# Kernel tuning notes

Hardware: AMD Instinct MI355X
Metric: run time of the kernel (lower is better)

The kernel has to match this reference:

```python
import jax, jax.numpy as jnp
import numpy as np

# geomloss SamplesLoss(loss='sinkhorn', p=2, blur=0.05):
#   cost C(x,y) = |x-y|^2 / 2, entropic eps = blur**p = 0.0025,
#   debiased divergence S = OT(x,y) - 0.5*OT(x,x) - 0.5*OT(y,y)
EPS = 0.05 ** 2          # blur**p
N_ITERS = 50             # fixed log-domain Sinkhorn iterations


def _cost(x, y):
    # x: [N,3], y: [M,3] -> [N,M] halved squared euclidean distance
    x2 = jnp.sum(x * x, axis=-1)
    y2 = jnp.sum(y * y, axis=-1)
    return 0.5 * (x2[:, None] + y2[None, :] - 2.0 * (x @ y.T))


def _ot_eps(x, y):
    # Entropic OT with uniform weights, log-domain Sinkhorn.
    N, M = x.shape[0], y.shape[0]
    logN = float(np.log(N))
    logM = float(np.log(M))
    C = _cost(x, y)  # [N,M]
    f0 = jnp.zeros((N,), dtype=x.dtype)
    g0 = jnp.zeros((M,), dtype=x.dtype)

    def step(carry, _):
        f, g = carry
        f = -EPS * (jax.nn.logsumexp((g[None, :] - C) / EPS, axis=1) - logM)
        g = -EPS * (jax.nn.logsumexp((f[:, None] - C) / EPS, axis=0) - logN)
        return (f, g), None

    (f, g), _ = jax.lax.scan(step, (f0, g0), None, length=N_ITERS)
    # OT cost at (approximate) optimal dual potentials
    return jnp.mean(f) + jnp.mean(g)


def _sinkhorn_div(x, y):
    # debiased Sinkhorn divergence per sample
    return _ot_eps(x, y) - 0.5 * _ot_eps(x, x) - 0.5 * _ot_eps(y, y)


def setup_inputs() -> dict:
    key = jax.random.key(0)
    k1, k2 = jax.random.split(key)
    B, N = 8, 2048
    pcs1 = jax.random.uniform(k1, (B, N, 3), dtype=jnp.float32)
    pcs2 = jax.random.uniform(k2, (B, N, 3), dtype=jnp.float32)
    return {"pcs1": pcs1, "pcs2": pcs2}


def reference(pcs1, pcs2):
    # mean over batch of per-sample Sinkhorn divergences
    losses = jax.vmap(_sinkhorn_div)(pcs1, pcs2)  # [B]
    return jnp.mean(losses)
```

## Files before the change

### kernel.cpp

```cpp
#include <hip/hip_runtime.h>

#ifndef __has_builtin
#define __has_builtin(x) 0
#endif

__device__ __forceinline__ float fexp2(float x) {
#if __has_builtin(__builtin_amdgcn_exp2f)
  return __builtin_amdgcn_exp2f(x);
#else
  return exp2f(x);
#endif
}
__device__ __forceinline__ float flog2(float x) {
#if __has_builtin(__builtin_amdgcn_logf)
  return __builtin_amdgcn_logf(x);
#else
  return log2f(x);
#endif
}

typedef float    f32x4 __attribute__((ext_vector_type(4)));
typedef unsigned int u32x2 __attribute__((ext_vector_type(2)));
typedef unsigned int u32x4 __attribute__((ext_vector_type(4)));
typedef _Float16 f16x4 __attribute__((ext_vector_type(4)));

__device__ __forceinline__ f32x4 mfma16x16x16(f16x4 a, f16x4 b, f32x4 c) {
#if __has_builtin(__builtin_amdgcn_mfma_f32_16x16x16_f16)
  return __builtin_amdgcn_mfma_f32_16x16x16_f16(a, b, c, 0, 0, 0);
#else
  return __builtin_amdgcn_mfma_f32_16x16x16f16(a, b, c, 0, 0, 0);
#endif
}

namespace {
constexpr int NPTS = 2048;
constexpr int NPROB = 24;
constexpr int THREADS = 512;
constexpr int NPASS = 100;
constexpr int PH = 512;
constexpr float KS  = 1.44269504088896340736f / 0.0025f;
constexpr float HKS = 0.5f * KS;
constexpr float NEG_EPS_LN2 = -0.0025f * 0.69314718055994530942f;
constexpr float LOG2N = 11.0f;
}

__device__ __forceinline__ void split2h(float v, float& h, float& m) {
  h = (float)(_Float16)v;
  m = (float)(_Float16)(v - h);
}
__device__ __forceinline__ void split3h(float v, float& h, float& m, float& l) {
  h = (float)(_Float16)v;
  float r1 = v - h;
  m = (float)(_Float16)r1;
  l = r1 - m;
}
__device__ __forceinline__ unsigned pkh(float a, float b) {
  unsigned short ab = __builtin_bit_cast(unsigned short, (_Float16)a);
  unsigned short bb = __builtin_bit_cast(unsigned short, (_Float16)b);
  return (unsigned)ab | ((unsigned)bb << 16);
}

__global__ void __launch_bounds__(256) sink_prep(
    const float* __restrict__ p1, const float* __restrict__ p2,
    u32x4* __restrict__ pre)
{
  const int g = blockIdx.x;
  const int set = g >> 3;
  const int j = (g & 7) * 256 + threadIdx.x;
  const float* src = (set < 8) ? p1 + set * (NPTS * 3)
                               : p2 + (set - 8) * (NPTS * 3);
  float sx = src[3 * j + 0], sy = src[3 * j + 1], sz = src[3 * j + 2];
  float q2 = HKS * (sx * sx + sy * sy + sz * sz);
  float shx, smx, shy, smy, shz, smz;
  split2h(KS * sx, shx, smx);
  split2h(KS * sy, shy, smy);
  split2h(KS * sz, shz, smz);
  pre[set * NPTS + j] =
      (u32x4){pkh(shx, smx), pkh(shy, smy), pkh(shz, smz), __float_as_uint(q2)};
}

template <bool PRE>
__global__ void __launch_bounds__(THREADS, 6) sink_mfma(
    const float* __restrict__ p1, const float* __restrict__ p2,
    float* __restrict__ fm, float* __restrict__ fs,
    float* __restrict__ gm, float* __restrict__ gs,
    const u32x4* __restrict__ pre, int t)
{
  __shared__ u32x4 Bfr[PH * 2];
  __shared__ float wmax[8];

  const int w   = blockIdx.x;
  const int p   = w >> 5;
  const int r_  = w & 31;
  const int blk = r_ & 15;
  const int h   = r_ >> 4;
  const int b    = p / 3;
  const int kind = p - 3 * b;
  const float* X = (kind == 2 ? p2 : p1) + b * (NPTS * 3);
  const float* Y = (kind == 1 ? p1 : p2) + b * (NPTS * 3);

  const bool even = (t & 1) == 0;
  const float* tgt = even ? X : Y;
  const float* src = even ? Y : X;
  const int sset = even ? (kind == 1 ? b : 8 + b) : (kind == 2 ? 8 + b : b);
  const u32x4* ps = pre + sset * NPTS;
  const float* pmA = even ? gm : fm;
  const float* psA = even ? gs : fs;
  float* omA = even ? fm : gm;
  float* osA = even ? fs : gs;

  const int tid  = threadIdx.x;
  const int lane = tid & 63;
  const int wv   = tid >> 6;
  const int l15  = lane & 15;
  const int kb   = lane >> 4;

  const int rowbase = blk * 128 + wv * 16;
  const int r = rowbase + l15;
  float tx = tgt[3 * r + 0], ty = tgt[3 * r + 1], tz = tgt[3 * r + 2];
  float thx, tmx, thy, tmy, thz, tmz;
  split2h(tx, thx, tmx);
  split2h(ty, thy, tmy);
  split2h(tz, thz, tmz);
  u32x2 areg;
  if (kb == 0)      { areg = (u32x2){pkh(thx, thx), pkh(tmx, tmx)}; }
  else if (kb == 1) { areg = (u32x2){pkh(thy, thy), pkh(tmy, tmy)}; }
  else if (kb == 2) { areg = (u32x2){pkh(thz, thz), pkh(tmz, tmz)}; }
  else              { areg = (u32x2){pkh(1.f, 1.f), pkh(1.f, 0.f)}; }
  const f16x4 afrag = __builtin_bit_cast(f16x4, areg);
  const float Bv = -HKS * (tx * tx + ty * ty + tz * tz);
  const float Bq0 = __shfl(Bv, kb * 4 + 0);
  const float Bq1 = __shfl(Bv, kb * 4 + 1);
  const float Bq2 = __shfl(Bv, kb * 4 + 2);
  const float Bq3 = __shfl(Bv, kb * 4 + 3);

  float Mx = -1e30f;
  float r0 = 0.f, r1 = 0.f, r2 = 0.f, r3 = 0.f;

  #pragma unroll
  for (int h2 = 0; h2 < 2; ++h2) {
    if (h2 == 1) __syncthreads();
    {
      int jl = tid;
      int jg = 1024 * h + PH * h2 + jl;
      float A, q2;
      u32x4 pv;
      if constexpr (PRE) {
        pv = ps[jg];
        q2 = __uint_as_float(pv.w);
      } else {
        float sx = src[3 * jg + 0], sy = src[3 * jg + 1], sz = src[3 * jg + 2];
        q2 = HKS * (sx * sx + sy * sy + sz * sz);
        float shx, smx, shy, smy, shz, smz;
        split2h(KS * sx, shx, smx);
        split2h(KS * sy, shy, smy);
        split2h(KS * sz, shz, smz);
        pv = (u32x4){pkh(shx, smx), pkh(shy, smy), pkh(shz, smz), 0u};
      }
      if (t == 0) {
        A = -q2;
      } else {
        float m0 = pmA[(p * 2 + 0) * NPTS + jg];
        float m1 = pmA[(p * 2 + 1) * NPTS + jg];
        float c0 = psA[(p * 2 + 0) * NPTS + jg];
        float c1 = psA[(p * 2 + 1) * NPTS + jg];
        float M = fmaxf(m0, m1);
        float S = fmaf(c0, fexp2(m0 - M), c1 * fexp2(m1 - M));
        A = LOG2N - M - flog2(fmaxf(S, 1e-38f));
      }
      float am = A + q2;
      float Ah, Am_, Al;
      split3h(A, Ah, Am_, Al);
      Bfr[jl * 2 + 0] = (u32x4){pv.x, pv.x, pv.y, pv.y};
      Bfr[jl * 2 + 1] = (u32x4){pv.z, pv.z, pkh(Ah, Am_), pkh(Al, 0.f)};
      #pragma unroll
      for (int off = 1; off <= 32; off <<= 1)
        am = fmaxf(am, __shfl_xor(am, off));
      if (lane == 0) wmax[wv] = am;
    }
    __syncthreads();

    const float Amax =
        fmaxf(fmaxf(fmaxf(wmax[0], wmax[1]), fmaxf(wmax[2], wmax[3])),
              fmaxf(fmaxf(wmax[4], wmax[5]), fmaxf(wmax[6], wmax[7])));
    const f32x4 cin = {Bq0 - Amax, Bq1 - Amax, Bq2 - Amax, Bq3 - Amax};

    const u32x2* bptr = (const u32x2*)Bfr + (l15 * 4 + kb);
    float s0 = 0.f, s1 = 0.f, s2 = 0.f, s3 = 0.f;
    #pragma unroll 4
    for (int tile = 0; tile < PH / 16; ++tile) {
      u32x2 braw = *bptr; bptr += 64;
      f16x4 bfrag = __builtin_bit_cast(f16x4, braw);
      f32x4 d = mfma16x16x16(afrag, bfrag, cin);
      s0 += fexp2(d.x);
      s1 += fexp2(d.y);
      s2 += fexp2(d.z);
      s3 += fexp2(d.w);
    }

    const float Mn = fmaxf(Mx, Amax);
    const float fo = fexp2(Mx - Mn);
    const float fn = fexp2(Amax - Mn);
    r0 = fmaf(r0, fo, s0 * fn);
    r1 = fmaf(r1, fo, s1 * fn);
    r2 = fmaf(r2, fo, s2 * fn);
    r3 = fmaf(r3, fo, s3 * fn);
    Mx = Mn;
  }

  #pragma unroll
  for (int off = 1; off <= 8; off <<= 1) {
    r0 += __shfl_xor(r0, off);
    r1 += __shfl_xor(r1, off);
    r2 += __shfl_xor(r2, off);
    r3 += __shfl_xor(r3, off);
  }

  if (l15 == 0) {
    float* om = omA + (p * 2 + h) * NPTS;
    float* os = osA + (p * 2 + h) * NPTS;
    int rr = rowbase + kb * 4;
    om[rr + 0] = Mx - Bq0; os[rr + 0] = r0;
    om[rr + 1] = Mx - Bq1; os[rr + 1] = r1;
    om[rr + 2] = Mx - Bq2; os[rr + 2] = r2;
    om[rr + 3] = Mx - Bq3; os[rr + 3] = r3;
  }
}

__global__ void __launch_bounds__(256) sink_partial(
    const float* __restrict__ fm, const float* __restrict__ fs,
    const float* __restrict__ gm, const float* __restrict__ gs,
    const float* __restrict__ p1, const float* __restrict__ p2,
    double* __restrict__ part)
{
  __shared__ double wsum[4];
  const int tid = threadIdx.x;
  const int blk = blockIdx.x;
  const int PER_SIDE = NPROB * NPTS;
  double acc = 0.0;
  #pragma unroll
  for (int k = 0; k < 4; ++k) {
    int idx = blk * 1024 + k * 256 + tid;
    int side = idx >= PER_SIDE;
    int rem  = idx - side * PER_SIDE;
    int p = rem >> 11;
    int i = rem & (NPTS - 1);
    const float* mA = side ? gm : fm;
    const float* sA = side ? gs : fs;
    float m0 = mA[(p * 2 + 0) * NPTS + i], m1 = mA[(p * 2 + 1) * NPTS + i];
    float c0 = sA[(p * 2 + 0) * NPTS + i], c1 = sA[(p * 2 + 1) * NPTS + i];
    float M = fmaxf(m0, m1);
    float S = fmaf(c0, fexp2(m0 - M), c1 * fexp2(m1 - M));
    int b = p / 3, kd = p - 3 * b;
    const float* rows = side ? (kd == 1 ? p1 : p2) : (kd == 2 ? p2 : p1);
    const float* pt = rows + b * (NPTS * 3) + 3 * i;
    float B = -HKS * (pt[0] * pt[0] + pt[1] * pt[1] + pt[2] * pt[2]);
    float val = NEG_EPS_LN2 * (M + B + flog2(fmaxf(S, 1e-38f)) - LOG2N);
    double wgt = (kd == 0) ? 1.0 : -0.5;
    acc += wgt * (double)val;
  }
  #pragma unroll
  for (int off = 1; off <= 32; off <<= 1) acc += __shfl_xor(acc, off);
  if ((tid & 63) == 0) wsum[tid >> 6] = acc;
  __syncthreads();
  if (tid == 0) part[blk] = ((wsum[0] + wsum[1]) + (wsum[2] + wsum[3]));
}

__global__ void __launch_bounds__(64) sink_reduce(
    const double* __restrict__ part, float* __restrict__ out)
{
  const int tid = threadIdx.x;
  double acc = part[tid] + (tid < 32 ? part[64 + tid] : 0.0);
  #pragma unroll
  for (int off = 1; off <= 32; off <<= 1) acc += __shfl_xor(acc, off);
  if (tid == 0) out[0] = (float)(acc / (8.0 * 2048.0));
}

extern "C" void kernel_launch(void* const* d_in, const int* in_sizes, int n_in,
                              void* d_out, int out_size, void* d_ws, size_t ws_size,
                              hipStream_t stream)
{
  const float* p1 = (const float*)d_in[0];
  const float* p2 = (const float*)d_in[1];
  const size_t elems = (size_t)NPROB * 2 * NPTS;
  float* fm = (float*)d_ws;
  float* fs = fm + elems;
  float* gm = fs + elems;
  float* gs = gm + elems;
  double* part = (double*)(gs + elems);
  u32x4* pre = (u32x4*)(part + 96);
  const size_t need_pre =
      4 * elems * sizeof(float) + 96 * sizeof(double) +
      (size_t)16 * NPTS * sizeof(u32x4);
  const bool use_pre = ws_size >= need_pre;

  if (use_pre) {
    sink_prep<<<dim3(128), dim3(256), 0, stream>>>(p1, p2, pre);
    for (int t = 0; t < NPASS; ++t)
      sink_mfma<true><<<dim3(NPROB * 32), dim3(THREADS), 0, stream>>>(
          p1, p2, fm, fs, gm, gs, pre, t);
  } else {
    for (int t = 0; t < NPASS; ++t)
      sink_mfma<false><<<dim3(NPROB * 32), dim3(THREADS), 0, stream>>>(
          p1, p2, fm, fs, gm, gs, pre, t);
  }
  sink_partial<<<dim3(96), dim3(256), 0, stream>>>(fm, fs, gm, gs, p1, p2, part);
  sink_reduce<<<dim3(1), dim3(64), 0, stream>>>(part, (float*)d_out);
}
```

Before: 1.705 ms.

## Double-buffer LDS tiles and prefetch second half potentials during first MFMA pass

Splits the two half-passes into explicit stages with separate LDS buffers, and issues the global loads for the second half's source points and dual potentials before the first MFMA/exp loop. This is meant to hide global load latency behind compute and remove one barrier between reuse of the shared buffer. It doubles LDS usage and lowers the launch-bounds occupancy hint from 6 to 3 blocks per CU, which allows more registers but may reduce latency hiding across waves.

```diff
diff --git a/kernel.cpp b/kernel.cpp
--- a/kernel.cpp
+++ b/kernel.cpp
@@ -37,6 +37,7 @@
 constexpr int NPROB = 24;
 constexpr int THREADS = 512;
 constexpr int NPASS = 100;
+constexpr int HALF = 1024;
 constexpr int PH = 512;
 constexpr float KS  = 1.44269504088896340736f / 0.0025f;
 constexpr float HKS = 0.5f * KS;
@@ -80,14 +81,14 @@
 }
 
 template <bool PRE>
-__global__ void __launch_bounds__(THREADS, 6) sink_mfma(
+__global__ void __launch_bounds__(THREADS, 3) sink_mfma(
     const float* __restrict__ p1, const float* __restrict__ p2,
     float* __restrict__ fm, float* __restrict__ fs,
     float* __restrict__ gm, float* __restrict__ gs,
     const u32x4* __restrict__ pre, int t)
 {
-  __shared__ u32x4 Bfr[PH * 2];
-  __shared__ float wmax[8];
+  __shared__ u32x4 Bfr[2][PH * 2];
+  __shared__ float wmax[2][8];
 
   const int w   = blockIdx.x;
   const int p   = w >> 5;
@@ -134,59 +135,118 @@
   const float Bq2 = __shfl(Bv, kb * 4 + 2);
   const float Bq3 = __shfl(Bv, kb * 4 + 3);
 
-  float Mx = -1e30f;
+  const int jl  = tid;
+  {
+    int jg = HALF * h + jl;
+    float A, q2;
+    u32x4 pv;
+    if constexpr (PRE) {
+      pv = ps[jg];
+      q2 = __uint_as_float(pv.w);
+    } else {
+      float sx = src[3 * jg + 0], sy = src[3 * jg + 1], sz = src[3 * jg + 2];
+      q2 = HKS * (sx * sx + sy * sy + sz * sz);
+      float shx, smx, shy, smy, shz, smz;
+      split2h(KS * sx, shx, smx);
+      split2h(KS * sy, shy, smy);
+      split2h(KS * sz, shz, smz);
+      pv = (u32x4){pkh(shx, smx), pkh(shy, smy), pkh(shz, smz), 0u};
+    }
+    if (t == 0) {
+      A = -q2;
+    } else {
+      float m0 = pmA[(p * 2 + 0) * NPTS + jg];
+      float m1 = pmA[(p * 2 + 1) * NPTS + jg];
+      float c0 = psA[(p * 2 + 0) * NPTS + jg];
+      float c1 = psA[(p * 2 + 1) * NPTS + jg];
+      float M = fmaxf(m0, m1);
+      float S = fmaf(c0, fexp2(m0 - M), c1 * fexp2(m1 - M));
+      A = LOG2N - M - flog2(fmaxf(S, 1e-38f));
+    }
+    float am = A + q2;
+    float Ah, Am_, Al;
+    split3h(A, Ah, Am_, Al);
+    Bfr[0][jl * 2 + 0] = (u32x4){pv.x, pv.x, pv.y, pv.y};
+    Bfr[0][jl * 2 + 1] = (u32x4){pv.z, pv.z, pkh(Ah, Am_), pkh(Al, 0.f)};
+    #pragma unroll
+    for (int off = 1; off <= 32; off <<= 1)
+      am = fmaxf(am, __shfl_xor(am, off));
+    if (lane == 0) wmax[0][wv] = am;
+  }
+  __syncthreads();
+
+  const int jg1 = HALF * h + PH + jl;
+  u32x4 pv1;
+  float sx1, sy1, sz1, q21;
+  if constexpr (PRE) {
+    pv1 = ps[jg1];
+    q21 = __uint_as_float(pv1.w);
+  } else {
+    sx1 = src[3 * jg1 + 0]; sy1 = src[3 * jg1 + 1]; sz1 = src[3 * jg1 + 2];
+  }
+  float pm0, pm1, pc0, pc1;
+  if (t > 0) {
+    pm0 = pmA[(p * 2 + 0) * NPTS + jg1];
+    pm1 = pmA[(p * 2 + 1) * NPTS + jg1];
+    pc0 = psA[(p * 2 + 0) * NPTS + jg1];
+    pc1 = psA[(p * 2 + 1) * NPTS + jg1];
+  }
+
+  const float Amax0 =
+      fmaxf(fmaxf(fmaxf(wmax[0][0], wmax[0][1]), fmaxf(wmax[0][2], wmax[0][3])),
+            fmaxf(fmaxf(wmax[0][4], wmax[0][5]), fmaxf(wmax[0][6], wmax[0][7])));
   float r0 = 0.f, r1 = 0.f, r2 = 0.f, r3 = 0.f;
-
-  #pragma unroll
-  for (int h2 = 0; h2 < 2; ++h2) {
-    if (h2 == 1) __syncthreads();
-    {
-      int jl = tid;
-      int jg = 1024 * h + PH * h2 + jl;
-      float A, q2;
-      u32x4 pv;
-      if constexpr (PRE) {
-        pv = ps[jg];
-        q2 = __uint_as_float(pv.w);
-      } else {
-        float sx = src[3 * jg + 0], sy = src[3 * jg + 1], sz = src[3 * jg + 2];
-        q2 = HKS * (sx * sx + sy * sy + sz * sz);
-        float shx, smx, shy, smy, shz, smz;
-        split2h(KS * sx, shx, smx);
-        split2h(KS * sy, shy, smy);
-        split2h(KS * sz, shz, smz);
-        pv = (u32x4){pkh(shx, smx), pkh(shy, smy), pkh(shz, smz), 0u};
-      }
-      if (t == 0) {
-        A = -q2;
-      } else {
-        float m0 = pmA[(p * 2 + 0) * NPTS + jg];
-        float m1 = pmA[(p * 2 + 1) * NPTS + jg];
-        float c0 = psA[(p * 2 + 0) * NPTS + jg];
-        float c1 = psA[(p * 2 + 1) * NPTS + jg];
-        float M = fmaxf(m0, m1);
-        float S = fmaf(c0, fexp2(m0 - M), c1 * fexp2(m1 - M));
-        A = LOG2N - M - flog2(fmaxf(S, 1e-38f));
-      }
-      float am = A + q2;
-      float Ah, Am_, Al;
-      split3h(A, Ah, Am_, Al);
-      Bfr[jl * 2 + 0] = (u32x4){pv.x, pv.x, pv.y, pv.y};
-      Bfr[jl * 2 + 1] = (u32x4){pv.z, pv.z, pkh(Ah, Am_), pkh(Al, 0.f)};
-      #pragma unroll
-      for (int off = 1; off <= 32; off <<= 1)
-        am = fmaxf(am, __shfl_xor(am, off));
-      if (lane == 0) wmax[wv] = am;
-    }
-    __syncthreads();
-
-    const float Amax =
-        fmaxf(fmaxf(fmaxf(wmax[0], wmax[1]), fmaxf(wmax[2], wmax[3])),
-              fmaxf(fmaxf(wmax[4], wmax[5]), fmaxf(wmax[6], wmax[7])));
-    const f32x4 cin = {Bq0 - Amax, Bq1 - Amax, Bq2 - Amax, Bq3 - Amax};
-
-    const u32x2* bptr = (const u32x2*)Bfr + (l15 * 4 + kb);
-    float s0 = 0.f, s1 = 0.f, s2 = 0.f, s3 = 0.f;
+  {
+    const f32x4 cin = {Bq0 - Amax0, Bq1 - Amax0, Bq2 - Amax0, Bq3 - Amax0};
+    const u32x2* bptr = (const u32x2*)Bfr[0] + (l15 * 4 + kb);
+    #pragma unroll 4
+    for (int tile = 0; tile < PH / 16; ++tile) {
+      u32x2 braw = *bptr; bptr += 64;
+      f16x4 bfrag = __builtin_bit_cast(f16x4, braw);
+      f32x4 d = mfma16x16x16(afrag, bfrag, cin);
+      r0 += fexp2(d.x);
+      r1 += fexp2(d.y);
+      r2 += fexp2(d.z);
+      r3 += fexp2(d.w);
+    }
+  }
+
+  {
+    if constexpr (!PRE) {
+      q21 = HKS * (sx1 * sx1 + sy1 * sy1 + sz1 * sz1);
+      float shx, smx, shy, smy, shz, smz;
+      split2h(KS * sx1, shx, smx);
+      split2h(KS * sy1, shy, smy);
+      split2h(KS * sz1, shz, smz);
+      pv1 = (u32x4){pkh(shx, smx), pkh(shy, smy), pkh(shz, smz), 0u};
+    }
+    float A;
+    if (t == 0) {
+      A = -q21;
+    } else {
+      float M = fmaxf(pm0, pm1);
+      float S = fmaf(pc0, fexp2(pm0 - M), pc1 * fexp2(pm1 - M));
+      A = LOG2N - M - flog2(fmaxf(S, 1e-38f));
+    }
+    float am = A + q21;
+    float Ah, Am_, Al;
+    split3h(A, Ah, Am_, Al);
+    Bfr[1][jl * 2 + 0] = (u32x4){pv1.x, pv1.x, pv1.y, pv1.y};
+    Bfr[1][jl * 2 + 1] = (u32x4){pv1.z, pv1.z, pkh(Ah, Am_), pkh(Al, 0.f)};
+    #pragma unroll
+    for (int off = 1; off <= 32; off <<= 1)
+      am = fmaxf(am, __shfl_xor(am, off));
+    if (lane == 0) wmax[1][wv] = am;
+  }
+  __syncthreads();
+
+  const float Amax1 =
+      fmaxf(fmaxf(fmaxf(wmax[1][0], wmax[1][1]), fmaxf(wmax[1][2], wmax[1][3])),
+            fmaxf(fmaxf(wmax[1][4], wmax[1][5]), fmaxf(wmax[1][6], wmax[1][7])));
+  float s0 = 0.f, s1 = 0.f, s2 = 0.f, s3 = 0.f;
+  {
+    const f32x4 cin = {Bq0 - Amax1, Bq1 - Amax1, Bq2 - Amax1, Bq3 - Amax1};
+    const u32x2* bptr = (const u32x2*)Bfr[1] + (l15 * 4 + kb);
     #pragma unroll 4
     for (int tile = 0; tile < PH / 16; ++tile) {
       u32x2 braw = *bptr; bptr += 64;
@@ -197,16 +257,15 @@
       s2 += fexp2(d.z);
       s3 += fexp2(d.w);
     }
-
-    const float Mn = fmaxf(Mx, Amax);
-    const float fo = fexp2(Mx - Mn);
-    const float fn = fexp2(Amax - Mn);
-    r0 = fmaf(r0, fo, s0 * fn);
-    r1 = fmaf(r1, fo, s1 * fn);
-    r2 = fmaf(r2, fo, s2 * fn);
-    r3 = fmaf(r3, fo, s3 * fn);
-    Mx = Mn;
-  }
+  }
+
+  const float Mx = fmaxf(Amax0, Amax1);
+  const float f0 = fexp2(Amax0 - Mx);
+  const float f1 = fexp2(Amax1 - Mx);
+  r0 = fmaf(r0, f0, s0 * f1);
+  r1 = fmaf(r1, f0, s1 * f1);
+  r2 = fmaf(r2, f0, s2 * f1);
+  r3 = fmaf(r3, f0, s3 * f1);
 
   #pragma unroll
   for (int off = 1; off <= 8; off <<= 1) {
```

After: 1.703 ms. About the same (-0.1%).
